# Kernel optimization log

Hardware: AMD Instinct MI355X
Metric: run time of the kernel (lower is better)

Reference implementation:

```python
import jax, jax.numpy as jnp
import numpy as np

N, E = 100000, 1600000
NODE_DIM, EDGE_DIM, HID = 128, 64, 128

def _mlp(x, w1, b1, w2, b2):
    # 2-layer MLP: Linear -> ReLU -> Linear (weights stored torch-style [out,in])
    return jax.nn.relu(x @ w1.T + b1) @ w2.T + b2

def setup_inputs() -> dict:
    key = jax.random.key(0)
    ks = jax.random.split(key, 24)
    g = lambda k, shp, fan: jax.random.normal(k, shp, jnp.float32) * (1.0 / np.sqrt(fan))
    return {
        "x": jax.random.normal(ks[0], (N, NODE_DIM), jnp.float32),
        "pos": jax.random.normal(ks[1], (N, 3), jnp.float32),
        "edge_index": jax.random.randint(ks[2], (2, E), 0, N),
        "edge_attr": jax.random.normal(ks[3], (E, EDGE_DIM), jnp.float32),
        # node_net: MLP(node_dim -> hid -> hid)
        "node_w1": g(ks[4], (HID, NODE_DIM), NODE_DIM), "node_b1": jnp.zeros((HID,), jnp.float32),
        "node_w2": g(ks[5], (HID, HID), HID), "node_b2": jnp.zeros((HID,), jnp.float32),
        # edge_net: MLP(edge_dim -> hid -> hid)
        "edge_w1": g(ks[6], (HID, EDGE_DIM), EDGE_DIM), "edge_b1": jnp.zeros((HID,), jnp.float32),
        "edge_w2": g(ks[7], (HID, HID), HID), "edge_b2": jnp.zeros((HID,), jnp.float32),
        # msg_net: Linear(hid, hid)
        "msg_w": g(ks[8], (HID, HID), HID), "msg_b": jnp.zeros((HID,), jnp.float32),
        # gate: MLP(edge_dim + node_dim -> hid -> hid)
        "gate_w1": g(ks[9], (HID, EDGE_DIM + NODE_DIM), EDGE_DIM + NODE_DIM), "gate_b1": jnp.zeros((HID,), jnp.float32),
        "gate_w2": g(ks[10], (HID, HID), HID), "gate_b2": jnp.zeros((HID,), jnp.float32),
        # centroid_lin: Linear(node_dim, hid)
        "cent_w": g(ks[11], (HID, NODE_DIM), NODE_DIM), "cent_b": jnp.zeros((HID,), jnp.float32),
        # layer norm
        "ln_g": jnp.ones((HID,), jnp.float32), "ln_b": jnp.zeros((HID,), jnp.float32),
        # out_transform: Linear(hid, node_dim)
        "out_w": g(ks[12], (NODE_DIM, HID), HID), "out_b": jnp.zeros((NODE_DIM,), jnp.float32),
    }

def reference(x, pos, edge_index, edge_attr,
              node_w1, node_b1, node_w2, node_b2,
              edge_w1, edge_b1, edge_w2, edge_b2,
              msg_w, msg_b,
              gate_w1, gate_b1, gate_w2, gate_b2,
              cent_w, cent_b, ln_g, ln_b, out_w, out_b):
    row, col = edge_index[0], edge_index[1]
    h_node = _mlp(x, node_w1, node_b1, node_w2, node_b2)          # (N, HID)
    h_edge = _mlp(edge_attr, edge_w1, edge_b1, edge_w2, edge_b2)   # (E, HID)
    msg_j = (h_edge * h_node[col]) @ msg_w.T + msg_b               # (E, HID)
    gate = _mlp(jnp.concatenate([edge_attr, x[col]], axis=-1),
                gate_w1, gate_b1, gate_w2, gate_b2)                # (E, HID)
    msg_j = msg_j * jax.nn.sigmoid(gate)
    aggr = jax.ops.segment_sum(msg_j, row, num_segments=x.shape[0])  # (N, HID)
    out = (x @ cent_w.T + cent_b) + aggr
    mu = jnp.mean(out, axis=-1, keepdims=True)
    var = jnp.var(out, axis=-1, keepdims=True)
    out = (out - mu) * jax.lax.rsqrt(var + 1e-5) * ln_g + ln_b
    return jax.nn.relu(out) @ out_w.T + out_b                      # (N, NODE_DIM)
```

## Files before the change

### kernel.cpp

```cpp
#include <hip/hip_runtime.h>

#define NN 100000
#define NE 1600000

typedef __bf16 bf16;
typedef bf16 bf16x8 __attribute__((ext_vector_type(8)));
typedef bf16 bf16x4 __attribute__((ext_vector_type(4)));
typedef float f32x4 __attribute__((ext_vector_type(4)));

__device__ __forceinline__ f32x4 mfma16(bf16x8 a, bf16x8 b, f32x4 c) {
    return __builtin_amdgcn_mfma_f32_16x16x32_bf16(a, b, c, 0, 0, 0);
}

__global__ void cvt_kernel(const float* __restrict__ s, bf16* __restrict__ d, int n4) {
    int i = blockIdx.x * 256 + threadIdx.x;
    if (i < n4) {
        f32x4 v = ((const f32x4*)s)[i];
        bf16x4 o;
        o[0] = (bf16)v[0]; o[1] = (bf16)v[1]; o[2] = (bf16)v[2]; o[3] = (bf16)v[3];
        ((bf16x4*)d)[i] = o;
    }
}

__launch_bounds__(256, 3)
__global__ void node_kernel(const bf16* __restrict__ xb,
                            const bf16* __restrict__ w1, const float* __restrict__ b1,
                            const bf16* __restrict__ w2, const float* __restrict__ b2,
                            const bf16* __restrict__ wc, const float* __restrict__ bc,
                            bf16* __restrict__ h_node, float* __restrict__ cent) {
    const int S = 136;
    __shared__ __align__(16) bf16 sX[64 * S];
    __shared__ __align__(16) bf16 sH[64 * S];
    const int tid = threadIdx.x;
    const int m0 = blockIdx.x * 64;
    {
        int e = tid >> 2, p = tid & 3;
        int gm = m0 + e;
        uint4 z = {0, 0, 0, 0};
        uint4* dst = (uint4*)(sX + e * S + p * 32);
        if (gm < NN) {
            const uint4* src = (const uint4*)(xb + (size_t)gm * 128 + p * 32);
#pragma unroll
            for (int j = 0; j < 4; ++j) dst[j] = src[j];
        } else {
#pragma unroll
            for (int j = 0; j < 4; ++j) dst[j] = z;
        }
    }
    __syncthreads();
    const int lane = tid & 63, wave = tid >> 6, t16 = lane & 15, quad = lane >> 4;
    const int n0 = wave * 32, koff = quad * 8;
    const f32x4 z4 = {0.f, 0.f, 0.f, 0.f};
    f32x4 acc[4][2];

#pragma unroll
    for (int mt = 0; mt < 4; ++mt) { acc[mt][0] = z4; acc[mt][1] = z4; }
#pragma unroll
    for (int ks = 0; ks < 4; ++ks) {
        bf16x8 bb0 = *(const bf16x8*)(w1 + (n0 + t16) * 128 + ks * 32 + koff);
        bf16x8 bb1 = *(const bf16x8*)(w1 + (n0 + 16 + t16) * 128 + ks * 32 + koff);
#pragma unroll
        for (int mt = 0; mt < 4; ++mt) {
            bf16x8 a = *(const bf16x8*)(sX + (mt * 16 + t16) * S + ks * 32 + koff);
            acc[mt][0] = mfma16(a, bb0, acc[mt][0]);
            acc[mt][1] = mfma16(a, bb1, acc[mt][1]);
        }
    }
    {
        float bi0 = b1[n0 + t16], bi1 = b1[n0 + 16 + t16];
#pragma unroll
        for (int mt = 0; mt < 4; ++mt)
#pragma unroll
            for (int nt = 0; nt < 2; ++nt) {
                int n = n0 + nt * 16 + t16;
                float bb = nt ? bi1 : bi0;
#pragma unroll
                for (int r = 0; r < 4; ++r) {
                    float v = acc[mt][nt][r] + bb;
                    sH[(mt * 16 + quad * 4 + r) * S + n] = (bf16)(v > 0.f ? v : 0.f);
                }
            }
    }
    __syncthreads();

#pragma unroll
    for (int mt = 0; mt < 4; ++mt) { acc[mt][0] = z4; acc[mt][1] = z4; }
#pragma unroll
    for (int ks = 0; ks < 4; ++ks) {
        bf16x8 bb0 = *(const bf16x8*)(w2 + (n0 + t16) * 128 + ks * 32 + koff);
        bf16x8 bb1 = *(const bf16x8*)(w2 + (n0 + 16 + t16) * 128 + ks * 32 + koff);
#pragma unroll
        for (int mt = 0; mt < 4; ++mt) {
            bf16x8 a = *(const bf16x8*)(sH + (mt * 16 + t16) * S + ks * 32 + koff);
            acc[mt][0] = mfma16(a, bb0, acc[mt][0]);
            acc[mt][1] = mfma16(a, bb1, acc[mt][1]);
        }
    }
    {
        float bi0 = b2[n0 + t16], bi1 = b2[n0 + 16 + t16];
#pragma unroll
        for (int mt = 0; mt < 4; ++mt)
#pragma unroll
            for (int nt = 0; nt < 2; ++nt) {
                int n = n0 + nt * 16 + t16;
                float bb = nt ? bi1 : bi0;
#pragma unroll
                for (int r = 0; r < 4; ++r) {
                    int gm = m0 + mt * 16 + quad * 4 + r;
                    if (gm < NN) h_node[(size_t)gm * 128 + n] = (bf16)(acc[mt][nt][r] + bb);
                }
            }
    }

#pragma unroll
    for (int mt = 0; mt < 4; ++mt) { acc[mt][0] = z4; acc[mt][1] = z4; }
#pragma unroll
    for (int ks = 0; ks < 4; ++ks) {
        bf16x8 bb0 = *(const bf16x8*)(wc + (n0 + t16) * 128 + ks * 32 + koff);
        bf16x8 bb1 = *(const bf16x8*)(wc + (n0 + 16 + t16) * 128 + ks * 32 + koff);
#pragma unroll
        for (int mt = 0; mt < 4; ++mt) {
            bf16x8 a = *(const bf16x8*)(sX + (mt * 16 + t16) * S + ks * 32 + koff);
            acc[mt][0] = mfma16(a, bb0, acc[mt][0]);
            acc[mt][1] = mfma16(a, bb1, acc[mt][1]);
        }
    }
    {
        float bi0 = bc[n0 + t16], bi1 = bc[n0 + 16 + t16];
#pragma unroll
        for (int mt = 0; mt < 4; ++mt)
#pragma unroll
            for (int nt = 0; nt < 2; ++nt) {
                int n = n0 + nt * 16 + t16;
                float bb = nt ? bi1 : bi0;
#pragma unroll
                for (int r = 0; r < 4; ++r) {
                    int gm = m0 + mt * 16 + quad * 4 + r;
                    if (gm < NN) cent[(size_t)gm * 128 + n] = acc[mt][nt][r] + bb;
                }
            }
    }
}

__launch_bounds__(256, 3)
__global__ void edge_kernel(const float* __restrict__ edge_attr,
                            const int* __restrict__ erow, const int* __restrict__ ecol,
                            const bf16* __restrict__ xb, const bf16* __restrict__ hnode,
                            const bf16* __restrict__ we1, const float* __restrict__ be1,
                            const bf16* __restrict__ we2, const float* __restrict__ be2,
                            const bf16* __restrict__ wm, const float* __restrict__ bm,
                            const bf16* __restrict__ wg1, const float* __restrict__ bg1,
                            const bf16* __restrict__ wg2, const float* __restrict__ bg2,
                            float* __restrict__ aggr) {
    const int SE = 72, S = 136;
    __shared__ __align__(16) bf16 sEA[64 * SE];
    __shared__ __align__(16) bf16 sX[64 * S];
    __shared__ __align__(16) bf16 sT[64 * S];
    __shared__ int rowS[64], colS[64];
    const int tid = threadIdx.x;
    const int e0 = blockIdx.x * 64;
    if (tid < 64) { rowS[tid] = erow[e0 + tid]; colS[tid] = ecol[e0 + tid]; }
    __syncthreads();
#pragma unroll
    for (int i = 0; i < 4; ++i) {
        int idx = tid * 4 + i * 1024;
        int e = idx >> 6, k = idx & 63;
        f32x4 v = *(const f32x4*)(edge_attr + (size_t)(e0 + e) * 64 + k);
        bf16x4 o;
        o[0] = (bf16)v[0]; o[1] = (bf16)v[1]; o[2] = (bf16)v[2]; o[3] = (bf16)v[3];
        *(bf16x4*)(sEA + e * SE + k) = o;
    }
    {
        int e = tid >> 2, p = tid & 3;
        const uint4* src = (const uint4*)(xb + (size_t)colS[e] * 128 + p * 32);
        uint4* dst = (uint4*)(sX + e * S + p * 32);
#pragma unroll
        for (int j = 0; j < 4; ++j) dst[j] = src[j];
    }
    __syncthreads();
    const int lane = tid & 63, wave = tid >> 6, t16 = lane & 15, quad = lane >> 4;
    const int n0 = wave * 32, koff = quad * 8;
    const f32x4 z4 = {0.f, 0.f, 0.f, 0.f};
    f32x4 acc[4][2];

#pragma unroll
    for (int mt = 0; mt < 4; ++mt) { acc[mt][0] = z4; acc[mt][1] = z4; }
#pragma unroll
    for (int ks = 0; ks < 2; ++ks) {
        bf16x8 bb0 = *(const bf16x8*)(wg1 + (n0 + t16) * 192 + ks * 32 + koff);
        bf16x8 bb1 = *(const bf16x8*)(wg1 + (n0 + 16 + t16) * 192 + ks * 32 + koff);
#pragma unroll
        for (int mt = 0; mt < 4; ++mt) {
            bf16x8 a = *(const bf16x8*)(sEA + (mt * 16 + t16) * SE + ks * 32 + koff);
            acc[mt][0] = mfma16(a, bb0, acc[mt][0]);
            acc[mt][1] = mfma16(a, bb1, acc[mt][1]);
        }
    }
#pragma unroll
    for (int ks = 0; ks < 4; ++ks) {
        bf16x8 bb0 = *(const bf16x8*)(wg1 + (n0 + t16) * 192 + 64 + ks * 32 + koff);
        bf16x8 bb1 = *(const bf16x8*)(wg1 + (n0 + 16 + t16) * 192 + 64 + ks * 32 + koff);
#pragma unroll
        for (int mt = 0; mt < 4; ++mt) {
            bf16x8 a = *(const bf16x8*)(sX + (mt * 16 + t16) * S + ks * 32 + koff);
            acc[mt][0] = mfma16(a, bb0, acc[mt][0]);
            acc[mt][1] = mfma16(a, bb1, acc[mt][1]);
        }
    }
    {
        float bi0 = bg1[n0 + t16], bi1 = bg1[n0 + 16 + t16];
#pragma unroll
        for (int mt = 0; mt < 4; ++mt)
#pragma unroll
            for (int nt = 0; nt < 2; ++nt) {
                int n = n0 + nt * 16 + t16;
                float bb = nt ? bi1 : bi0;
#pragma unroll
                for (int r = 0; r < 4; ++r) {
                    float v = acc[mt][nt][r] + bb;
                    sT[(mt * 16 + quad * 4 + r) * S + n] = (bf16)(v > 0.f ? v : 0.f);
                }
            }
    }
    __syncthreads();

    uint4 hreg[4];
    {
        int e = tid >> 2, p = tid & 3;
        const uint4* src = (const uint4*)(hnode + (size_t)colS[e] * 128 + p * 32);
#pragma unroll
        for (int j = 0; j < 4; ++j) hreg[j] = src[j];
    }

#pragma unroll
    for (int mt = 0; mt < 4; ++mt) { acc[mt][0] = z4; acc[mt][1] = z4; }
#pragma unroll
    for (int ks = 0; ks < 4; ++ks) {
        bf16x8 bb0 = *(const bf16x8*)(wg2 + (n0 + t16) * 128 + ks * 32 + koff);
        bf16x8 bb1 = *(const bf16x8*)(wg2 + (n0 + 16 + t16) * 128 + ks * 32 + koff);
#pragma unroll
        for (int mt = 0; mt < 4; ++mt) {
            bf16x8 a = *(const bf16x8*)(sT + (mt * 16 + t16) * S + ks * 32 + koff);
            acc[mt][0] = mfma16(a, bb0, acc[mt][0]);
            acc[mt][1] = mfma16(a, bb1, acc[mt][1]);
        }
    }
    f32x4 gsig[4][2];
    {
        float bi0 = bg2[n0 + t16], bi1 = bg2[n0 + 16 + t16];
#pragma unroll
        for (int mt = 0; mt < 4; ++mt)
#pragma unroll
            for (int nt = 0; nt < 2; ++nt) {
                float bb = nt ? bi1 : bi0;
#pragma unroll
                for (int r = 0; r < 4; ++r) {
                    float v = acc[mt][nt][r] + bb;
                    gsig[mt][nt][r] = 1.f / (1.f + __expf(-v));
                }
            }
    }
    {
        int e = tid >> 2, p = tid & 3;
        uint4* dst = (uint4*)(sX + e * S + p * 32);
#pragma unroll
        for (int j = 0; j < 4; ++j) dst[j] = hreg[j];
    }
    __syncthreads();

#pragma unroll
    for (int mt = 0; mt < 4; ++mt) { acc[mt][0] = z4; acc[mt][1] = z4; }
#pragma unroll
    for (int ks = 0; ks < 2; ++ks) {
        bf16x8 bb0 = *(const bf16x8*)(we1 + (n0 + t16) * 64 + ks * 32 + koff);
        bf16x8 bb1 = *(const bf16x8*)(we1 + (n0 + 16 + t16) * 64 + ks * 32 + koff);
#pragma unroll
        for (int mt = 0; mt < 4; ++mt) {
            bf16x8 a = *(const bf16x8*)(sEA + (mt * 16 + t16) * SE + ks * 32 + koff);
            acc[mt][0] = mfma16(a, bb0, acc[mt][0]);
            acc[mt][1] = mfma16(a, bb1, acc[mt][1]);
        }
    }
    {
        float bi0 = be1[n0 + t16], bi1 = be1[n0 + 16 + t16];
#pragma unroll
        for (int mt = 0; mt < 4; ++mt)
#pragma unroll
            for (int nt = 0; nt < 2; ++nt) {
                int n = n0 + nt * 16 + t16;
                float bb = nt ? bi1 : bi0;
#pragma unroll
                for (int r = 0; r < 4; ++r) {
                    float v = acc[mt][nt][r] + bb;
                    sT[(mt * 16 + quad * 4 + r) * S + n] = (bf16)(v > 0.f ? v : 0.f);
                }
            }
    }
    __syncthreads();

#pragma unroll
    for (int mt = 0; mt < 4; ++mt) { acc[mt][0] = z4; acc[mt][1] = z4; }
#pragma unroll
    for (int ks = 0; ks < 4; ++ks) {
        bf16x8 bb0 = *(const bf16x8*)(we2 + (n0 + t16) * 128 + ks * 32 + koff);
        bf16x8 bb1 = *(const bf16x8*)(we2 + (n0 + 16 + t16) * 128 + ks * 32 + koff);
#pragma unroll
        for (int mt = 0; mt < 4; ++mt) {
            bf16x8 a = *(const bf16x8*)(sT + (mt * 16 + t16) * S + ks * 32 + koff);
            acc[mt][0] = mfma16(a, bb0, acc[mt][0]);
            acc[mt][1] = mfma16(a, bb1, acc[mt][1]);
        }
    }
    {
        float bi0 = be2[n0 + t16], bi1 = be2[n0 + 16 + t16];
#pragma unroll
        for (int mt = 0; mt < 4; ++mt)
#pragma unroll
            for (int nt = 0; nt < 2; ++nt) {
                int n = n0 + nt * 16 + t16;
                float bb = nt ? bi1 : bi0;
#pragma unroll
                for (int r = 0; r < 4; ++r) {
                    float v = acc[mt][nt][r] + bb;
                    float hv = (float)sX[(mt * 16 + quad * 4 + r) * S + n];
                    acc[mt][nt][r] = v * hv;
                }
            }
    }
    __syncthreads();
#pragma unroll
    for (int mt = 0; mt < 4; ++mt)
#pragma unroll
        for (int nt = 0; nt < 2; ++nt) {
            int n = n0 + nt * 16 + t16;
#pragma unroll
            for (int r = 0; r < 4; ++r) {
                float p = acc[mt][nt][r];
                bf16 hi = (bf16)p;
                sT[(mt * 16 + quad * 4 + r) * S + n] = hi;
                sX[(mt * 16 + quad * 4 + r) * S + n] = (bf16)(p - (float)hi);
            }
        }
    __syncthreads();

#pragma unroll
    for (int mt = 0; mt < 4; ++mt) { acc[mt][0] = z4; acc[mt][1] = z4; }
#pragma unroll
    for (int ks = 0; ks < 4; ++ks) {
        bf16x8 bb0 = *(const bf16x8*)(wm + (n0 + t16) * 128 + ks * 32 + koff);
        bf16x8 bb1 = *(const bf16x8*)(wm + (n0 + 16 + t16) * 128 + ks * 32 + koff);
#pragma unroll
        for (int mt = 0; mt < 4; ++mt) {
            bf16x8 a = *(const bf16x8*)(sT + (mt * 16 + t16) * S + ks * 32 + koff);
            acc[mt][0] = mfma16(a, bb0, acc[mt][0]);
            acc[mt][1] = mfma16(a, bb1, acc[mt][1]);
        }
    }
#pragma unroll
    for (int ks = 0; ks < 4; ++ks) {
        bf16x8 bb0 = *(const bf16x8*)(wm + (n0 + t16) * 128 + ks * 32 + koff);
        bf16x8 bb1 = *(const bf16x8*)(wm + (n0 + 16 + t16) * 128 + ks * 32 + koff);
#pragma unroll
        for (int mt = 0; mt < 4; ++mt) {
            bf16x8 a = *(const bf16x8*)(sX + (mt * 16 + t16) * S + ks * 32 + koff);
            acc[mt][0] = mfma16(a, bb0, acc[mt][0]);
            acc[mt][1] = mfma16(a, bb1, acc[mt][1]);
        }
    }
    {
        float bi0 = bm[n0 + t16], bi1 = bm[n0 + 16 + t16];
#pragma unroll
        for (int mt = 0; mt < 4; ++mt)
#pragma unroll
            for (int nt = 0; nt < 2; ++nt) {
                int n = n0 + nt * 16 + t16;
                float bb = nt ? bi1 : bi0;
#pragma unroll
                for (int r = 0; r < 4; ++r) {
                    int mloc = mt * 16 + quad * 4 + r;
                    float v = (acc[mt][nt][r] + bb) * gsig[mt][nt][r];
                    atomicAdd(aggr + (size_t)rowS[mloc] * 128 + n, v);
                }
            }
    }
}

__launch_bounds__(256, 3)
__global__ void final_kernel(const float* __restrict__ cent, const float* __restrict__ aggr,
                             const float* __restrict__ lng, const float* __restrict__ lnb,
                             const bf16* __restrict__ wo, const float* __restrict__ bo,
                             float* __restrict__ out) {
    const int S = 136;
    __shared__ __align__(16) bf16 sA[128 * S];
    const int tid = threadIdx.x;
    const int m0 = blockIdx.x * 128;
    {
        int r = tid >> 1, h = tid & 1;
        int gm = m0 + r;
        f32x4 vb[16];
        float sum = 0.f, sq = 0.f;
        if (gm < NN) {
            const f32x4* c4 = (const f32x4*)(cent + (size_t)gm * 128 + h * 64);
            const f32x4* a4 = (const f32x4*)(aggr + (size_t)gm * 128 + h * 64);
#pragma unroll
            for (int j = 0; j < 16; ++j) {
                f32x4 v = c4[j] + a4[j];
                vb[j] = v;
                sum += v[0] + v[1] + v[2] + v[3];
                sq += v[0] * v[0] + v[1] * v[1] + v[2] * v[2] + v[3] * v[3];
            }
        } else {
            f32x4 z = {0.f, 0.f, 0.f, 0.f};
#pragma unroll
            for (int j = 0; j < 16; ++j) vb[j] = z;
        }
        sum += __shfl_xor(sum, 1);
        sq += __shfl_xor(sq, 1);
        float mu = sum * (1.f / 128.f);
        float var = sq * (1.f / 128.f) - mu * mu;
        float rs = rsqrtf(var + 1e-5f);
#pragma unroll
        for (int j = 0; j < 16; ++j) {
            bf16x4 o;
#pragma unroll
            for (int c = 0; c < 4; ++c) {
                int k = h * 64 + j * 4 + c;
                float y = (vb[j][c] - mu) * rs * lng[k] + lnb[k];
                y = y > 0.f ? y : 0.f;
                o[c] = (bf16)(gm < NN ? y : 0.f);
            }
            *(bf16x4*)(sA + r * S + h * 64 + j * 4) = o;
        }
    }
    __syncthreads();
    const int lane = tid & 63, wave = tid >> 6, t16 = lane & 15, quad = lane >> 4;
    const int n0 = wave * 32, koff = quad * 8;
    const f32x4 z4 = {0.f, 0.f, 0.f, 0.f};
    f32x4 acc[8][2];
#pragma unroll
    for (int mt = 0; mt < 8; ++mt) { acc[mt][0] = z4; acc[mt][1] = z4; }
#pragma unroll
    for (int ks = 0; ks < 4; ++ks) {
        bf16x8 bb0 = *(const bf16x8*)(wo + (n0 + t16) * 128 + ks * 32 + koff);
        bf16x8 bb1 = *(const bf16x8*)(wo + (n0 + 16 + t16) * 128 + ks * 32 + koff);
#pragma unroll
        for (int mt = 0; mt < 8; ++mt) {
            bf16x8 a = *(const bf16x8*)(sA + (mt * 16 + t16) * S + ks * 32 + koff);
            acc[mt][0] = mfma16(a, bb0, acc[mt][0]);
            acc[mt][1] = mfma16(a, bb1, acc[mt][1]);
        }
    }
    {
        float bi0 = bo[n0 + t16], bi1 = bo[n0 + 16 + t16];
#pragma unroll
        for (int mt = 0; mt < 8; ++mt)
#pragma unroll
            for (int nt = 0; nt < 2; ++nt) {
                int n = n0 + nt * 16 + t16;
                float bb = nt ? bi1 : bi0;
#pragma unroll
                for (int r = 0; r < 4; ++r) {
                    int gm = m0 + mt * 16 + quad * 4 + r;
                    if (gm < NN) out[(size_t)gm * 128 + n] = acc[mt][nt][r] + bb;
                }
            }
    }
}

extern "C" void kernel_launch(void* const* d_in, const int* in_sizes, int n_in,
                              void* d_out, int out_size, void* d_ws, size_t ws_size,
                              hipStream_t stream) {
    bf16* wsb = (bf16*)d_ws;
    bf16* nw1 = wsb + 0;
    bf16* nw2 = wsb + 16384;
    bf16* cw = wsb + 32768;
    bf16* ew1 = wsb + 49152;
    bf16* ew2 = wsb + 57344;
    bf16* mw = wsb + 73728;
    bf16* gw1 = wsb + 90112;
    bf16* gw2 = wsb + 114688;
    bf16* ow = wsb + 131072;
    bf16* xb = wsb + 147456;
    bf16* hb = xb + (size_t)NN * 128;
    float* cent = (float*)(hb + (size_t)NN * 128);
    float* aggr = cent + (size_t)NN * 128;

    auto cv = [&](int idx, bf16* dst, int n) {
        cvt_kernel<<<(n / 4 + 255) / 256, 256, 0, stream>>>((const float*)d_in[idx], dst, n / 4);
    };
    cv(4, nw1, 16384);
    cv(6, nw2, 16384);
    cv(18, cw, 16384);
    cv(8, ew1, 8192);
    cv(10, ew2, 16384);
    cv(12, mw, 16384);
    cv(14, gw1, 24576);
    cv(16, gw2, 16384);
    cv(22, ow, 16384);
    cv(0, xb, NN * 128);
    hipMemsetAsync(aggr, 0, (size_t)NN * 128 * sizeof(float), stream);

    node_kernel<<<(NN + 63) / 64, 256, 0, stream>>>(
        xb, nw1, (const float*)d_in[5], nw2, (const float*)d_in[7],
        cw, (const float*)d_in[19], hb, cent);

    const int* ei = (const int*)d_in[2];
    edge_kernel<<<NE / 64, 256, 0, stream>>>(
        (const float*)d_in[3], ei, ei + NE, xb, hb,
        ew1, (const float*)d_in[9], ew2, (const float*)d_in[11],
        mw, (const float*)d_in[13], gw1, (const float*)d_in[15],
        gw2, (const float*)d_in[17], aggr);

    final_kernel<<<(NN + 127) / 128, 256, 0, stream>>>(
        cent, aggr, (const float*)d_in[20], (const float*)d_in[21],
        ow, (const float*)d_in[23], (float*)d_out);
}
```

Baseline: 1.447 ms.

## Precompute x-part of gate layer-1 per node and gather it per edge

The gate MLP's first layer is linear in concat(edge_attr, x[col]), so the x[col] contribution is now computed once per node in node_kernel (x @ Wg1[:,64:]^T) and stored as an fp32 buffer gx. The edge kernel gathers gx rows per edge instead of gathering x and running a K=128 MFMA, which cuts per-edge matrix work by 4 MFMA k-steps. It also loads h_node directly into shared memory up front and overlaps the gate layer-2 and edge layer-1 MMAs, removing a barrier and register staging. In exchange the per-edge gather is now scattered fp32 scalar loads (twice the bytes of bf16 x rows and poorly coalesced), and node_kernel does extra work and writes a 51 MB buffer.

```diff
diff --git a/kernel.cpp b/kernel.cpp
--- a/kernel.cpp
+++ b/kernel.cpp
@@ -27,7 +27,9 @@
                             const bf16* __restrict__ w1, const float* __restrict__ b1,
                             const bf16* __restrict__ w2, const float* __restrict__ b2,
                             const bf16* __restrict__ wc, const float* __restrict__ bc,
-                            bf16* __restrict__ h_node, float* __restrict__ cent) {
+                            const bf16* __restrict__ wg1,
+                            bf16* __restrict__ h_node, float* __restrict__ cent,
+                            float* __restrict__ gx) {
     const int S = 136;
     __shared__ __align__(16) bf16 sX[64 * S];
     __shared__ __align__(16) bf16 sH[64 * S];
@@ -140,12 +142,37 @@
                 }
             }
     }
+
+#pragma unroll
+    for (int mt = 0; mt < 4; ++mt) { acc[mt][0] = z4; acc[mt][1] = z4; }
+#pragma unroll
+    for (int ks = 0; ks < 4; ++ks) {
+        bf16x8 bb0 = *(const bf16x8*)(wg1 + (n0 + t16) * 192 + 64 + ks * 32 + koff);
+        bf16x8 bb1 = *(const bf16x8*)(wg1 + (n0 + 16 + t16) * 192 + 64 + ks * 32 + koff);
+#pragma unroll
+        for (int mt = 0; mt < 4; ++mt) {
+            bf16x8 a = *(const bf16x8*)(sX + (mt * 16 + t16) * S + ks * 32 + koff);
+            acc[mt][0] = mfma16(a, bb0, acc[mt][0]);
+            acc[mt][1] = mfma16(a, bb1, acc[mt][1]);
+        }
+    }
+#pragma unroll
+    for (int mt = 0; mt < 4; ++mt)
+#pragma unroll
+        for (int nt = 0; nt < 2; ++nt) {
+            int n = n0 + nt * 16 + t16;
+#pragma unroll
+            for (int r = 0; r < 4; ++r) {
+                int gm = m0 + mt * 16 + quad * 4 + r;
+                if (gm < NN) gx[(size_t)gm * 128 + n] = acc[mt][nt][r];
+            }
+        }
 }
 
 __launch_bounds__(256, 3)
 __global__ void edge_kernel(const float* __restrict__ edge_attr,
                             const int* __restrict__ erow, const int* __restrict__ ecol,
-                            const bf16* __restrict__ xb, const bf16* __restrict__ hnode,
+                            const bf16* __restrict__ hnode, const float* __restrict__ gx,
                             const bf16* __restrict__ we1, const float* __restrict__ be1,
                             const bf16* __restrict__ we2, const float* __restrict__ be2,
                             const bf16* __restrict__ wm, const float* __restrict__ bm,
@@ -172,7 +199,7 @@
     }
     {
         int e = tid >> 2, p = tid & 3;
-        const uint4* src = (const uint4*)(xb + (size_t)colS[e] * 128 + p * 32);
+        const uint4* src = (const uint4*)(hnode + (size_t)colS[e] * 128 + p * 32);
         uint4* dst = (uint4*)(sX + e * S + p * 32);
 #pragma unroll
         for (int j = 0; j < 4; ++j) dst[j] = src[j];
@@ -183,6 +210,15 @@
     const f32x4 z4 = {0.f, 0.f, 0.f, 0.f};
     f32x4 acc[4][2];
 
+    float gval[4][2][4];
+#pragma unroll
+    for (int mt = 0; mt < 4; ++mt)
+#pragma unroll
+        for (int r = 0; r < 4; ++r) {
+            const float* grow = gx + (size_t)colS[mt * 16 + quad * 4 + r] * 128;
+            gval[mt][0][r] = grow[n0 + t16];
+            gval[mt][1][r] = grow[n0 + 16 + t16];
+        }
 #pragma unroll
     for (int mt = 0; mt < 4; ++mt) { acc[mt][0] = z4; acc[mt][1] = z4; }
 #pragma unroll
@@ -196,17 +232,6 @@
             acc[mt][1] = mfma16(a, bb1, acc[mt][1]);
         }
     }
-#pragma unroll
-    for (int ks = 0; ks < 4; ++ks) {
-        bf16x8 bb0 = *(const bf16x8*)(wg1 + (n0 + t16) * 192 + 64 + ks * 32 + koff);
-        bf16x8 bb1 = *(const bf16x8*)(wg1 + (n0 + 16 + t16) * 192 + 64 + ks * 32 + koff);
-#pragma unroll
-        for (int mt = 0; mt < 4; ++mt) {
-            bf16x8 a = *(const bf16x8*)(sX + (mt * 16 + t16) * S + ks * 32 + koff);
-            acc[mt][0] = mfma16(a, bb0, acc[mt][0]);
-            acc[mt][1] = mfma16(a, bb1, acc[mt][1]);
-        }
-    }
     {
         float bi0 = bg1[n0 + t16], bi1 = bg1[n0 + 16 + t16];
 #pragma unroll
@@ -217,23 +242,16 @@
                 float bb = nt ? bi1 : bi0;
 #pragma unroll
                 for (int r = 0; r < 4; ++r) {
-                    float v = acc[mt][nt][r] + bb;
+                    float v = acc[mt][nt][r] + bb + gval[mt][nt][r];
                     sT[(mt * 16 + quad * 4 + r) * S + n] = (bf16)(v > 0.f ? v : 0.f);
                 }
             }
     }
     __syncthreads();
 
-    uint4 hreg[4];
-    {
-        int e = tid >> 2, p = tid & 3;
-        const uint4* src = (const uint4*)(hnode + (size_t)colS[e] * 128 + p * 32);
-#pragma unroll
-        for (int j = 0; j < 4; ++j) hreg[j] = src[j];
-    }
-
-#pragma unroll
-    for (int mt = 0; mt < 4; ++mt) { acc[mt][0] = z4; acc[mt][1] = z4; }
+    f32x4 gsig[4][2];
+#pragma unroll
+    for (int mt = 0; mt < 4; ++mt) { gsig[mt][0] = z4; gsig[mt][1] = z4; acc[mt][0] = z4; acc[mt][1] = z4; }
 #pragma unroll
     for (int ks = 0; ks < 4; ++ks) {
         bf16x8 bb0 = *(const bf16x8*)(wg2 + (n0 + t16) * 128 + ks * 32 + koff);
@@ -241,35 +259,10 @@
 #pragma unroll
         for (int mt = 0; mt < 4; ++mt) {
             bf16x8 a = *(const bf16x8*)(sT + (mt * 16 + t16) * S + ks * 32 + koff);
-            acc[mt][0] = mfma16(a, bb0, acc[mt][0]);
-            acc[mt][1] = mfma16(a, bb1, acc[mt][1]);
-        }
-    }
-    f32x4 gsig[4][2];
-    {
-        float bi0 = bg2[n0 + t16], bi1 = bg2[n0 + 16 + t16];
-#pragma unroll
-        for (int mt = 0; mt < 4; ++mt)
-#pragma unroll
-            for (int nt = 0; nt < 2; ++nt) {
-                float bb = nt ? bi1 : bi0;
-#pragma unroll
-                for (int r = 0; r < 4; ++r) {
-                    float v = acc[mt][nt][r] + bb;
-                    gsig[mt][nt][r] = 1.f / (1.f + __expf(-v));
-                }
-            }
-    }
-    {
-        int e = tid >> 2, p = tid & 3;
-        uint4* dst = (uint4*)(sX + e * S + p * 32);
-#pragma unroll
-        for (int j = 0; j < 4; ++j) dst[j] = hreg[j];
-    }
-    __syncthreads();
-
-#pragma unroll
-    for (int mt = 0; mt < 4; ++mt) { acc[mt][0] = z4; acc[mt][1] = z4; }
+            gsig[mt][0] = mfma16(a, bb0, gsig[mt][0]);
+            gsig[mt][1] = mfma16(a, bb1, gsig[mt][1]);
+        }
+    }
 #pragma unroll
     for (int ks = 0; ks < 2; ++ks) {
         bf16x8 bb0 = *(const bf16x8*)(we1 + (n0 + t16) * 64 + ks * 32 + koff);
@@ -280,6 +273,21 @@
             acc[mt][0] = mfma16(a, bb0, acc[mt][0]);
             acc[mt][1] = mfma16(a, bb1, acc[mt][1]);
         }
+    }
+    __syncthreads();
+    {
+        float bi0 = bg2[n0 + t16], bi1 = bg2[n0 + 16 + t16];
+#pragma unroll
+        for (int mt = 0; mt < 4; ++mt)
+#pragma unroll
+            for (int nt = 0; nt < 2; ++nt) {
+                float bb = nt ? bi1 : bi0;
+#pragma unroll
+                for (int r = 0; r < 4; ++r) {
+                    float v = gsig[mt][nt][r] + bb;
+                    gsig[mt][nt][r] = 1.f / (1.f + __expf(-v));
+                }
+            }
     }
     {
         float bi0 = be1[n0 + t16], bi1 = be1[n0 + 16 + t16];
@@ -484,6 +492,7 @@
     bf16* hb = xb + (size_t)NN * 128;
     float* cent = (float*)(hb + (size_t)NN * 128);
     float* aggr = cent + (size_t)NN * 128;
+    float* gx = aggr + (size_t)NN * 128;
 
     auto cv = [&](int idx, bf16* dst, int n) {
         cvt_kernel<<<(n / 4 + 255) / 256, 256, 0, stream>>>((const float*)d_in[idx], dst, n / 4);
@@ -502,11 +511,11 @@
 
     node_kernel<<<(NN + 63) / 64, 256, 0, stream>>>(
         xb, nw1, (const float*)d_in[5], nw2, (const float*)d_in[7],
-        cw, (const float*)d_in[19], hb, cent);
+        cw, (const float*)d_in[19], gw1, hb, cent, gx);
 
     const int* ei = (const int*)d_in[2];
     edge_kernel<<<NE / 64, 256, 0, stream>>>(
-        (const float*)d_in[3], ei, ei + NE, xb, hb,
+        (const float*)d_in[3], ei, ei + NE, hb, gx,
         ew1, (const float*)d_in[9], ew2, (const float*)d_in[11],
         mw, (const float*)d_in[13], gw1, (const float*)d_in[15],
         gw2, (const float*)d_in[17], aggr);
```

New measurement: 1.402 ms. 1.03x faster.
